# Kernel tuning notes

Hardware: AMD Instinct MI355X
Metric: run time of the kernel (lower is better)

The kernel has to match this reference:

```python
import jax, jax.numpy as jnp
import numpy as np

N_NODES = 50000
N_EDGES = 800000


def setup_inputs() -> dict:
    key = jax.random.key(0)
    ks = jax.random.split(key, 8)
    x = jax.random.normal(ks[0], (N_NODES, 128), dtype=jnp.float32)
    edge_src = jax.random.randint(ks[1], (N_EDGES,), 0, N_NODES, dtype=jnp.int32)
    edge_dst = jax.random.randint(ks[2], (N_EDGES,), 0, N_NODES, dtype=jnp.int32)
    # normalized-adjacency-style positive edge weights
    edge_weight = jax.random.uniform(ks[3], (N_EDGES,), dtype=jnp.float32)
    # Kipf-style uniform(-stdv, stdv) init, stdv = 1/sqrt(fan_out)
    def w(k, fi, fo):
        stdv = 1.0 / np.sqrt(fo)
        return jax.random.uniform(k, (fi, fo), minval=-stdv, maxval=stdv, dtype=jnp.float32)
    W1 = w(ks[4], 128, 128)
    W2 = w(ks[5], 128, 128)
    W3 = w(ks[6], 128, 64)
    b1 = jnp.zeros((128,), jnp.float32)
    b2 = jnp.zeros((128,), jnp.float32)
    b3 = jnp.zeros((64,), jnp.float32)
    return {"x": x, "edge_src": edge_src, "edge_dst": edge_dst,
            "edge_weight": edge_weight, "W1": W1, "b1": b1,
            "W2": W2, "b2": b2, "W3": W3, "b3": b3}


def reference(x, edge_src, edge_dst, edge_weight, W1, b1, W2, b2, W3, b3):
    N = x.shape[0]

    def graph_conv(h, W, b):
        # support = h @ W  (dense GEMM)
        support = h @ W
        # spmm(adj, support): gather source rows, scale by edge weight,
        # scatter-add into destination rows
        msg = edge_weight[:, None] * support[edge_src]          # [E, d_out]
        agg = jax.ops.segment_sum(msg, edge_dst, num_segments=N)
        return agg + b

    h = jax.nn.relu(graph_conv(x, W1, b1))
    h = jax.nn.relu(graph_conv(h, W2, b2))
    h = graph_conv(h, W3, b3)
    return jax.nn.log_softmax(h, axis=1)
```

## Files before the change

kernel.cpp:

```cpp
#include <hip/hip_runtime.h>
#include <cstdint>
#include <cstddef>

typedef __attribute__((ext_vector_type(8))) short short8v;
typedef __attribute__((ext_vector_type(4))) float f32x4;

__device__ inline uint bf16_rne(float f) {
    uint u = __float_as_uint(f);
    return (u + 0x7fffu + ((u >> 16) & 1u)) >> 16;
}
__device__ inline float bf16lo_to_f(uint v) { return __uint_as_float(v << 16); }
__device__ inline float bf16hi_to_f(uint v) { return __uint_as_float(v & 0xffff0000u); }

#define MAXDEG 64

__device__ inline void pack_one(const float* __restrict__ W, ushort* __restrict__ Wp,
                                int NC, int i) {
    int j = i & 7, l = (i >> 3) & 63, kb = (i >> 9) & 3, c = i >> 11;
    int row = kb * 32 + ((l >> 4) & 3) * 8 + j;
    int col = c * 16 + (l & 15);
    Wp[i] = (ushort)bf16_rne(W[row * NC + col]);
}

__global__ void init_kernel(int* __restrict__ cnt, int N,
                            const float* __restrict__ W1, ushort* __restrict__ Wp1,
                            const float* __restrict__ W2, ushort* __restrict__ Wp2,
                            const float* __restrict__ W3, ushort* __restrict__ Wp3) {
    int i = blockIdx.x * blockDim.x + threadIdx.x;
    if (i < N) cnt[i] = 0;
    int zblocks = (N + 255) >> 8;
    int p = i - zblocks * 256;
    if (p >= 0) {
        if (p < 16384) pack_one(W1, Wp1, 128, p);
        else if (p < 32768) pack_one(W2, Wp2, 128, p - 16384);
        else if (p < 40960) pack_one(W3, Wp3, 64, p - 32768);
    }
}

template <int NC, bool F32IN>
__device__ __forceinline__ void gemm_body(const void* __restrict__ Xin,
                                          const ushort* __restrict__ Wp,
                                          ushort* __restrict__ Out, int M, int bid,
                                          ushort* WL) {
    const int t = threadIdx.x;
    {
        const uint4* srcp = (const uint4*)Wp;
        uint4* dstp = (uint4*)WL;
#pragma unroll
        for (int i = 0; i < NC / 16; ++i) dstp[t + i * 256] = srcp[t + i * 256];
    }
    __syncthreads();

    const int wave = t >> 6, l = t & 63;
    const int lr = l & 15, lh = l >> 4;
    const int rowbase = bid * 64 + wave * 16;
    const int arow_idx = min(rowbase + lr, M - 1);

    short8v a[4];
    if (F32IN) {
        const float* arow = (const float*)Xin + (size_t)arow_idx * 128 + lh * 8;
#pragma unroll
        for (int kb = 0; kb < 4; ++kb) {
            float4 u = *(const float4*)(arow + kb * 32);
            float4 v = *(const float4*)(arow + kb * 32 + 4);
            short8v av;
            av[0] = (short)bf16_rne(u.x); av[1] = (short)bf16_rne(u.y);
            av[2] = (short)bf16_rne(u.z); av[3] = (short)bf16_rne(u.w);
            av[4] = (short)bf16_rne(v.x); av[5] = (short)bf16_rne(v.y);
            av[6] = (short)bf16_rne(v.z); av[7] = (short)bf16_rne(v.w);
            a[kb] = av;
        }
    } else {
        const ushort* arow = (const ushort*)Xin + (size_t)arow_idx * 128 + lh * 8;
#pragma unroll
        for (int kb = 0; kb < 4; ++kb) a[kb] = *(const short8v*)(arow + kb * 32);
    }

    f32x4 acc[NC / 16];
#pragma unroll
    for (int c = 0; c < NC / 16; ++c) acc[c] = (f32x4){0.f, 0.f, 0.f, 0.f};

#pragma unroll
    for (int c = 0; c < NC / 16; ++c)
#pragma unroll
        for (int kb = 0; kb < 4; ++kb) {
            short8v b = *(const short8v*)(WL + ((c * 4 + kb) * 64 + l) * 8);
            acc[c] = __builtin_amdgcn_mfma_f32_16x16x32_bf16(a[kb], b, acc[c], 0, 0, 0);
        }

#pragma unroll
    for (int c = 0; c < NC / 16; ++c)
#pragma unroll
        for (int i = 0; i < 4; ++i) {
            int row = rowbase + lh * 4 + i;
            if (row < M) Out[(size_t)row * NC + c * 16 + lr] = (ushort)bf16_rne(acc[c][i]);
        }
}

template <int NC, bool F32IN>
__global__ __launch_bounds__(256) void gemm_mfma(const void* __restrict__ Xin,
                                                 const ushort* __restrict__ Wp,
                                                 ushort* __restrict__ Out, int M) {
    __shared__ ushort WL[128 * NC];
    gemm_body<NC, F32IN>(Xin, Wp, Out, M, blockIdx.x, WL);
}

__global__ __launch_bounds__(256) void gemm1_fill_kernel(
        const float* __restrict__ X, const ushort* __restrict__ Wp1,
        ushort* __restrict__ Out, int M, int GB, int T,
        const int* __restrict__ esrc, const int* __restrict__ edst,
        const float* __restrict__ ew,
        int* __restrict__ cnt, uint* __restrict__ slots, int E) {
    __shared__ ushort WL[128 * 128];
    const int b = blockIdx.x;
    const int R = max(1, T / GB);
    if ((b % R == 0) && (b / R < GB)) {
        gemm_body<128, true>(X, Wp1, Out, M, b / R, WL);
        return;
    }
    const int ngemm_before = min((b + R - 1) / R, GB);
    const int q = (b - ngemm_before) * 256 + threadIdx.x;
    if (q < E) {
        int dv = edst[q];
        int p = atomicAdd(&cnt[dv], 1);
        if (p < MAXDEG)
            slots[(size_t)dv * MAXDEG + p] = (bf16_rne(ew[q]) << 16) | (uint)esrc[q];
    }
}

__global__ void spmm128_kernel(const uint* __restrict__ S, const int* __restrict__ cnt,
                               const uint* __restrict__ slots, const float* __restrict__ bias,
                               uint* __restrict__ Out, int N) {
    const int node = blockIdx.x * (blockDim.x >> 6) + (threadIdx.x >> 6);
    const int lane = threadIdx.x & 63;
    if (node >= N) return;
    const int e1 = min(cnt[node], MAXDEG);
    const uint* sl = slots + (size_t)node * MAXDEG;
    float ax = 0.f, ay = 0.f;
    int e = 0;

#define EDGE128(pk)                                                  \
    {                                                                \
        uint _p = (pk);                                              \
        float _w = __uint_as_float(_p & 0xffff0000u);                \
        uint _v = S[(size_t)(_p & 0xffffu) * 64 + lane];             \
        ax = fmaf(_w, bf16lo_to_f(_v), ax);                          \
        ay = fmaf(_w, bf16hi_to_f(_v), ay);                          \
    }

    for (; e + 8 <= e1; e += 8) {
        uint4 c0 = *(const uint4*)(sl + e);
        uint4 c1 = *(const uint4*)(sl + e + 4);
        EDGE128(c0.x); EDGE128(c0.y); EDGE128(c0.z); EDGE128(c0.w);
        EDGE128(c1.x); EDGE128(c1.y); EDGE128(c1.z); EDGE128(c1.w);
    }
    for (; e + 4 <= e1; e += 4) {
        uint4 c0 = *(const uint4*)(sl + e);
        EDGE128(c0.x); EDGE128(c0.y); EDGE128(c0.z); EDGE128(c0.w);
    }
    for (; e < e1; ++e) EDGE128(sl[e]);
#undef EDGE128

    float2 bv = ((const float2*)bias)[lane];
    ax = fmaxf(ax + bv.x, 0.f);
    ay = fmaxf(ay + bv.y, 0.f);
    Out[(size_t)node * 64 + lane] = (bf16_rne(ay) << 16) | bf16_rne(ax);
}

__global__ void spmm64_kernel(const uint* __restrict__ S32, const int* __restrict__ cnt,
                              const uint* __restrict__ slots, const float* __restrict__ bias,
                              float* __restrict__ Out, int N) {
    const int node = blockIdx.x * (blockDim.x >> 5) + (threadIdx.x >> 5);
    const int l = threadIdx.x & 31;
    if (node >= N) return;
    const int e1 = min(cnt[node], MAXDEG);
    const uint* sl = slots + (size_t)node * MAXDEG;
    float a0 = 0.f, a1 = 0.f;
    int e = 0;

#define EDGE64(pk)                                                  \
    {                                                               \
        uint _p = (pk);                                             \
        float _w = __uint_as_float(_p & 0xffff0000u);               \
        uint _v = S32[(size_t)(_p & 0xffffu) * 32 + l];             \
        a0 = fmaf(_w, bf16lo_to_f(_v), a0);                         \
        a1 = fmaf(_w, bf16hi_to_f(_v), a1);                         \
    }

    for (; e + 8 <= e1; e += 8) {
        uint4 c0 = *(const uint4*)(sl + e);
        uint4 c1 = *(const uint4*)(sl + e + 4);
        EDGE64(c0.x); EDGE64(c0.y); EDGE64(c0.z); EDGE64(c0.w);
        EDGE64(c1.x); EDGE64(c1.y); EDGE64(c1.z); EDGE64(c1.w);
    }
    for (; e + 4 <= e1; e += 4) {
        uint4 c0 = *(const uint4*)(sl + e);
        EDGE64(c0.x); EDGE64(c0.y); EDGE64(c0.z); EDGE64(c0.w);
    }
    for (; e < e1; ++e) EDGE64(sl[e]);
#undef EDGE64

    float2 bv = ((const float2*)bias)[l];
    float v0 = a0 + bv.x;
    float v1 = a1 + bv.y;
    float m = fmaxf(v0, v1);
#pragma unroll
    for (int d = 16; d >= 1; d >>= 1) m = fmaxf(m, __shfl_xor(m, d));
    float s = __expf(v0 - m) + __expf(v1 - m);
#pragma unroll
    for (int d = 16; d >= 1; d >>= 1) s += __shfl_xor(s, d);
    float ls = __logf(s);
    float2 o;
    o.x = (v0 - m) - ls;
    o.y = (v1 - m) - ls;
    ((float2*)Out)[(size_t)node * 32 + l] = o;
}


extern "C" void kernel_launch(void* const* d_in, const int* in_sizes, int n_in,
                              void* d_out, int out_size, void* d_ws, size_t ws_size,
                              hipStream_t stream) {
    const float* x  = (const float*)d_in[0];
    const int* esrc = (const int*)d_in[1];
    const int* edst = (const int*)d_in[2];
    const float* ew = (const float*)d_in[3];
    const float* W1 = (const float*)d_in[4];
    const float* b1 = (const float*)d_in[5];
    const float* W2 = (const float*)d_in[6];
    const float* b2 = (const float*)d_in[7];
    const float* W3 = (const float*)d_in[8];
    const float* b3 = (const float*)d_in[9];

    const int N = in_sizes[0] / 128;
    const int E = in_sizes[1];

    char* ws = (char*)d_ws;
    auto alloc = [&](size_t bytes) {
        char* p = ws;
        ws += (bytes + 255) & ~(size_t)255;
        return p;
    };
    int* cnt     = (int*)alloc((size_t)N * 4);
    uint* slots  = (uint*)alloc((size_t)N * MAXDEG * 4);
    ushort* Sb   = (ushort*)alloc((size_t)N * 128 * 2);
    ushort* Hb   = (ushort*)alloc((size_t)N * 128 * 2);
    ushort* Wp1  = (ushort*)alloc(128 * 128 * 2);
    ushort* Wp2  = (ushort*)alloc(128 * 128 * 2);
    ushort* Wp3  = (ushort*)alloc(128 * 64 * 2);
    (void)ws_size;

    const int zblocks = (N + 255) / 256;
    init_kernel<<<zblocks + (40960 + 255) / 256, 256, 0, stream>>>(
        cnt, N, W1, Wp1, W2, Wp2, W3, Wp3);

    const int GB = (N + 63) / 64;
    const int FB = (E + 255) / 256;
    gemm1_fill_kernel<<<GB + FB, 256, 0, stream>>>(
        x, Wp1, Sb, N, GB, GB + FB, esrc, edst, ew, cnt, slots, E);

    spmm128_kernel<<<(N + 3) / 4, 256, 0, stream>>>((const uint*)Sb, cnt, slots, b1, (uint*)Hb, N);

    gemm_mfma<128, false><<<GB, 256, 0, stream>>>(Hb, Wp2, Sb, N);
    spmm128_kernel<<<(N + 3) / 4, 256, 0, stream>>>((const uint*)Sb, cnt, slots, b2, (uint*)Hb, N);

    gemm_mfma<64, false><<<GB, 256, 0, stream>>>(Hb, Wp3, Sb, N);
    spmm64_kernel<<<(N + 7) / 8, 256, 0, stream>>>((const uint*)Sb, cnt, slots, b3, (float*)d_out, N);
}
```

Baseline: 185.7 us.

## Bucket edge-slot fill by destination range across 8-block groups

Fill blocks are now grouped in sets of 8. Each block in a group scans the same edge chunk, reading destinations as int4, but only inserts edges whose destination falls in its own eighth of the node range. The aim is to keep atomics and slot writes for a given block within a smaller address region, improving L2/locality, likely tied to the 8 XCDs on MI355X. The cost is that every edge's destination is read eight times, and the GEMM block index mapping is reworked to match. A tail loop handles the E%4 leftover edges. GEMM tiles with index of GB or more are presumably guarded inside gemm_body.

```diff
diff --git a/kernel.cpp b/kernel.cpp
--- a/kernel.cpp
+++ b/kernel.cpp
@@ -107,25 +107,54 @@
 
 __global__ __launch_bounds__(256) void gemm1_fill_kernel(
         const float* __restrict__ X, const ushort* __restrict__ Wp1,
-        ushort* __restrict__ Out, int M, int GB, int T,
+        ushort* __restrict__ Out, int M, int GG, int TG,
         const int* __restrict__ esrc, const int* __restrict__ edst,
         const float* __restrict__ ew,
-        int* __restrict__ cnt, uint* __restrict__ slots, int E) {
+        int* __restrict__ cnt, uint* __restrict__ slots, int E, int N) {
     __shared__ ushort WL[128 * 128];
-    const int b = blockIdx.x;
-    const int R = max(1, T / GB);
-    if ((b % R == 0) && (b / R < GB)) {
-        gemm_body<128, true>(X, Wp1, Out, M, b / R, WL);
+    const int g = blockIdx.x >> 3;
+    const int i = blockIdx.x & 7;
+    const int R = max(1, TG / GG);
+    if ((g % R == 0) && (g / R < GG)) {
+        gemm_body<128, true>(X, Wp1, Out, M, (g / R) * 8 + i, WL);
         return;
     }
-    const int ngemm_before = min((b + R - 1) / R, GB);
-    const int q = (b - ngemm_before) * 256 + threadIdx.x;
-    if (q < E) {
-        int dv = edst[q];
-        int p = atomicAdd(&cnt[dv], 1);
-        if (p < MAXDEG)
-            slots[(size_t)dv * MAXDEG + p] = (bf16_rne(ew[q]) << 16) | (uint)esrc[q];
-    }
+    const int gemm_before = min((g + R - 1) / R, GG);
+    const int fg = g - gemm_before;
+    const int NFG = TG - GG;
+    const int bucket = i;
+    const int lo = (int)((long)bucket * N / 8);
+    const int hi = (int)((long)(bucket + 1) * N / 8);
+    const unsigned range = (unsigned)(hi - lo);
+
+    const int E4 = E >> 2;
+    const int chunk = (E4 + NFG - 1) / NFG;
+    const int b4 = fg * chunk;
+    const int e4 = min(E4, b4 + chunk);
+    const int4* dst4 = (const int4*)edst;
+
+#define FILL_ONE(idx, dv)                                                        \
+    if ((unsigned)((dv) - lo) < range) {                                         \
+        int p = atomicAdd(&cnt[dv], 1);                                          \
+        if (p < MAXDEG)                                                          \
+            slots[(size_t)(dv) * MAXDEG + p] =                                   \
+                (bf16_rne(ew[idx]) << 16) | (uint)esrc[idx];                     \
+    }
+
+    for (int q = b4 + threadIdx.x; q < e4; q += 256) {
+        int4 d = dst4[q];
+        int idx = q * 4;
+        FILL_ONE(idx + 0, d.x);
+        FILL_ONE(idx + 1, d.y);
+        FILL_ONE(idx + 2, d.z);
+        FILL_ONE(idx + 3, d.w);
+    }
+    if (fg == 0 && threadIdx.x < (unsigned)(E & 3)) {
+        int idx = (E & ~3) + threadIdx.x;
+        int dv = edst[idx];
+        FILL_ONE(idx, dv);
+    }
+#undef FILL_ONE
 }
 
 __global__ void spmm128_kernel(const uint* __restrict__ S, const int* __restrict__ cnt,
@@ -254,9 +283,11 @@
         cnt, N, W1, Wp1, W2, Wp2, W3, Wp3);
 
     const int GB = (N + 63) / 64;
-    const int FB = (E + 255) / 256;
-    gemm1_fill_kernel<<<GB + FB, 256, 0, stream>>>(
-        x, Wp1, Sb, N, GB, GB + FB, esrc, edst, ew, cnt, slots, E);
+    const int GG = (GB + 7) / 8;
+    const int NFG = 256;
+    const int TG = GG + NFG;
+    gemm1_fill_kernel<<<TG * 8, 256, 0, stream>>>(
+        x, Wp1, Sb, N, GG, TG, esrc, edst, ew, cnt, slots, E, N);
 
     spmm128_kernel<<<(N + 3) / 4, 256, 0, stream>>>((const uint*)Sb, cnt, slots, b1, (uint*)Hb, N);
 
```

After: 165.6 us. 10.8% less time.

## Bucket edges by destination range before scattering into adjacency slots

Applied to the files above, without the earlier changes.

Edge-to-slot construction becomes two passes. First, edges are partitioned into 8 destination-range buckets using block-local counters and one global atomic per bucket, interleaved with the first GEMM. Then a separate scatter kernel walks each bucket and does the per-node atomics and slot writes. The goal is better locality for the cnt atomics and slot writes, since each bucket covers a compact node range that may stay in cache. The cost is an extra kernel launch and an intermediate buffer aliased onto Hb. Each bucket is capped at 131072 entries, and packing 16-bit src and dst fields into one word assumes N ≤ 65536.

```diff
diff --git a/kernel.cpp b/kernel.cpp
--- a/kernel.cpp
+++ b/kernel.cpp
@@ -13,6 +13,7 @@
 __device__ inline float bf16hi_to_f(uint v) { return __uint_as_float(v & 0xffff0000u); }
 
 #define MAXDEG 64
+#define CAP 131072
 
 __device__ inline void pack_one(const float* __restrict__ W, ushort* __restrict__ Wp,
                                 int NC, int i) {
@@ -22,12 +23,13 @@
     Wp[i] = (ushort)bf16_rne(W[row * NC + col]);
 }
 
-__global__ void init_kernel(int* __restrict__ cnt, int N,
+__global__ void init_kernel(int* __restrict__ cnt, int* __restrict__ pcnt, int N,
                             const float* __restrict__ W1, ushort* __restrict__ Wp1,
                             const float* __restrict__ W2, ushort* __restrict__ Wp2,
                             const float* __restrict__ W3, ushort* __restrict__ Wp3) {
     int i = blockIdx.x * blockDim.x + threadIdx.x;
     if (i < N) cnt[i] = 0;
+    if (i < 8) pcnt[i] = 0;
     int zblocks = (N + 255) >> 8;
     int p = i - zblocks * 256;
     if (p >= 0) {
@@ -105,26 +107,73 @@
     gemm_body<NC, F32IN>(Xin, Wp, Out, M, blockIdx.x, WL);
 }
 
-__global__ __launch_bounds__(256) void gemm1_fill_kernel(
+__global__ __launch_bounds__(256) void gemm1_part_kernel(
         const float* __restrict__ X, const ushort* __restrict__ Wp1,
-        ushort* __restrict__ Out, int M, int GB, int T,
+        ushort* __restrict__ Out, int M, int GG, int NFG, int TG,
         const int* __restrict__ esrc, const int* __restrict__ edst,
         const float* __restrict__ ew,
-        int* __restrict__ cnt, uint* __restrict__ slots, int E) {
+        int* __restrict__ pcnt, int2* __restrict__ part, int E, int N) {
     __shared__ ushort WL[128 * 128];
-    const int b = blockIdx.x;
-    const int R = max(1, T / GB);
-    if ((b % R == 0) && (b / R < GB)) {
-        gemm_body<128, true>(X, Wp1, Out, M, b / R, WL);
+    const int g = blockIdx.x >> 3;
+    const int i = blockIdx.x & 7;
+    const int S = max(1, TG / NFG);
+    const bool is_fill = (g % S == 0) && (g / S < NFG);
+    if (!is_fill) {
+        const int fills_before = min((g + S - 1) / S, NFG);
+        gemm_body<128, true>(X, Wp1, Out, M, (g - fills_before) * 8 + i, WL);
         return;
     }
-    const int ngemm_before = min((b + R - 1) / R, GB);
-    const int q = (b - ngemm_before) * 256 + threadIdx.x;
-    if (q < E) {
-        int dv = edst[q];
-        int p = atomicAdd(&cnt[dv], 1);
-        if (p < MAXDEG)
-            slots[(size_t)dv * MAXDEG + p] = (bf16_rne(ew[q]) << 16) | (uint)esrc[q];
+    const int fb = (g / S) * 8 + i;
+    __shared__ int lcnt[8];
+    __shared__ int gbase[8];
+    if (threadIdx.x < 8) lcnt[threadIdx.x] = 0;
+    __syncthreads();
+
+    const int base = fb * 2048;
+    int bj[8], rj[8];
+    int2 rec[8];
+#pragma unroll
+    for (int j = 0; j < 8; ++j) {
+        int idx = base + j * 256 + threadIdx.x;
+        bj[j] = -1;
+        if (idx < E) {
+            int dv = edst[idx];
+            int b = (int)(((long)dv * 8) / N);
+            bj[j] = b;
+            rj[j] = atomicAdd(&lcnt[b], 1);
+            rec[j].x = (dv << 16) | esrc[idx];
+            rec[j].y = __float_as_int(ew[idx]);
+        }
+    }
+    __syncthreads();
+    if (threadIdx.x < 8)
+        gbase[threadIdx.x] = atomicAdd(&pcnt[threadIdx.x], lcnt[threadIdx.x]);
+    __syncthreads();
+#pragma unroll
+    for (int j = 0; j < 8; ++j) {
+        if (bj[j] >= 0) {
+            int gpos = gbase[bj[j]] + rj[j];
+            if (gpos < CAP) part[(size_t)bj[j] * CAP + gpos] = rec[j];
+        }
+    }
+}
+
+__global__ __launch_bounds__(256) void scatter_kernel(
+        const int* __restrict__ pcnt, const int2* __restrict__ part,
+        int* __restrict__ cnt, uint* __restrict__ slots) {
+    const int bucket = blockIdx.x & 7;
+    const int slice = blockIdx.x >> 3;
+    const int nsl = gridDim.x >> 3;
+    const int nb = min(pcnt[bucket], CAP);
+    const int2* p = part + (size_t)bucket * CAP;
+    for (int q = slice * 256 + threadIdx.x; q < nb; q += nsl * 256) {
+        int2 r = p[q];
+        uint dv = (uint)r.x >> 16;
+        uint src = (uint)r.x & 0xffffu;
+        int pos = atomicAdd(&cnt[dv], 1);
+        if (pos < MAXDEG)
+            slots[(size_t)dv * MAXDEG + pos] =
+                (bf16_rne(__int_as_float(r.y)) << 16) | src;
     }
 }
 
@@ -241,6 +290,7 @@
         return p;
     };
     int* cnt     = (int*)alloc((size_t)N * 4);
+    int* pcnt    = (int*)alloc(8 * 4);
     uint* slots  = (uint*)alloc((size_t)N * MAXDEG * 4);
     ushort* Sb   = (ushort*)alloc((size_t)N * 128 * 2);
     ushort* Hb   = (ushort*)alloc((size_t)N * 128 * 2);
@@ -248,15 +298,21 @@
     ushort* Wp2  = (ushort*)alloc(128 * 128 * 2);
     ushort* Wp3  = (ushort*)alloc(128 * 64 * 2);
     (void)ws_size;
+    int2* part = (int2*)Hb;
 
     const int zblocks = (N + 255) / 256;
     init_kernel<<<zblocks + (40960 + 255) / 256, 256, 0, stream>>>(
-        cnt, N, W1, Wp1, W2, Wp2, W3, Wp3);
+        cnt, pcnt, N, W1, Wp1, W2, Wp2, W3, Wp3);
 
     const int GB = (N + 63) / 64;
-    const int FB = (E + 255) / 256;
-    gemm1_fill_kernel<<<GB + FB, 256, 0, stream>>>(
-        x, Wp1, Sb, N, GB, GB + FB, esrc, edst, ew, cnt, slots, E);
+    const int GG = (GB + 7) / 8;
+    const int NFB = (E + 2047) / 2048;
+    const int NFG = (NFB + 7) / 8;
+    const int TG = GG + NFG;
+    gemm1_part_kernel<<<TG * 8, 256, 0, stream>>>(
+        x, Wp1, Sb, N, GG, NFG, TG, esrc, edst, ew, pcnt, part, E, N);
+
+    scatter_kernel<<<64 * 8, 256, 0, stream>>>(pcnt, part, cnt, slots);
 
     spmm128_kernel<<<(N + 3) / 4, 256, 0, stream>>>((const uint*)Sb, cnt, slots, b1, (uint*)Hb, N);
 
```

New measurement: 170.3 us. -8.3%, faster.
